# Kernel optimization log

Measured on AMD Instinct MI355X. Metric: run time of the kernel, lower is better.

Reference implementation:

```python
import jax, jax.numpy as jnp
import numpy as np

B, IN, OUT, E, CTX, DEMO = 32768, 512, 128, 16, 256, 16
HID = IN // 2
GATE_IN = CTX + IN + DEMO  # 784


def setup_inputs() -> dict:
    key = jax.random.key(0)
    ks = jax.random.split(key, 9)
    inp = {
        'x': jax.random.normal(ks[0], (B, IN), dtype=jnp.float32),
        'u': jax.random.normal(ks[1], (B, CTX), dtype=jnp.float32),
        'd': jax.random.normal(ks[2], (B, DEMO), dtype=jnp.float32),
        # gate Linear(GATE_IN -> E)
        'gate_W': jax.random.normal(ks[3], (E, GATE_IN), dtype=jnp.float32) * 0.02,
        'gate_b': jnp.zeros((E,), dtype=jnp.float32),
        # per-expert MLP: Linear(IN->HID), ReLU, Linear(HID->OUT); stacked over experts
        'W1': jax.random.normal(ks[4], (E, HID, IN), dtype=jnp.float32) * 0.02,
        'b1': jnp.zeros((E, HID), dtype=jnp.float32),
        'W2': jax.random.normal(ks[5], (E, OUT, HID), dtype=jnp.float32) * 0.02,
        'b2': jnp.zeros((E, OUT), dtype=jnp.float32),
    }
    return inp


def reference(x, u, d, gate_W, gate_b, W1, b1, W2, b2):
    # gate input = cat([u, x, d], dim=1)  -> [B, GATE_IN]
    g_in = jnp.concatenate([u, x, d], axis=1)
    gate_logits = g_in @ gate_W.T + gate_b            # [B, E]
    weights = jax.nn.softmax(gate_logits, axis=1)     # [B, E]
    # all-expert MLP as batched GEMMs
    h = jax.nn.relu(jnp.einsum('bi,ehi->beh', x, W1) + b1[None])   # [B, E, HID]
    expert_outputs = jnp.einsum('beh,eoh->beo', h, W2) + b2[None]  # [B, E, OUT]
    # mixture_mode == 'logits': weighted sum over experts
    out = jnp.einsum('be,beo->bo', weights, expert_outputs)        # [B, OUT]
    return out
```

## Files before the change

### kernel.cpp

```cpp
#include <hip/hip_runtime.h>

#define B_    32768
#define IN_   512
#define HID_  256
#define OUT_  128
#define E_    16
#define CTX_  256
#define DEMO_ 16
#define GIN_  784

typedef __attribute__((ext_vector_type(8))) short short8;
typedef __attribute__((ext_vector_type(4))) float floatx4;

__device__ __forceinline__ short f2bf(float x){
  unsigned u = __builtin_bit_cast(unsigned, x);
  u += 0x7FFFu + ((u >> 16) & 1u);
  return (short)(u >> 16);
}

__device__ __forceinline__ short8 pack8(float4 a, float4 b){
  short8 r;
  r[0]=f2bf(a.x); r[1]=f2bf(a.y); r[2]=f2bf(a.z); r[3]=f2bf(a.w);
  r[4]=f2bf(b.x); r[5]=f2bf(b.y); r[6]=f2bf(b.z); r[7]=f2bf(b.w);
  return r;
}

__device__ __forceinline__ void load_lds16(const short* g, short* l){
  __builtin_amdgcn_global_load_lds((const __attribute__((address_space(1))) void*)g,
                                   (__attribute__((address_space(3))) void*)l,
                                   16, 0, 0);
}

#define VMCNT8()  asm volatile("s_waitcnt vmcnt(8)"  ::: "memory")
#define VMCNT0()  asm volatile("s_waitcnt vmcnt(0)"  ::: "memory")
#define BAR() do{ asm volatile("" ::: "memory"); __builtin_amdgcn_s_barrier(); \
                  asm volatile("" ::: "memory"); }while(0)
#define LGKM0() do{ asm volatile("s_waitcnt lgkmcnt(0)" ::: "memory"); \
                    __builtin_amdgcn_sched_barrier(0); }while(0)

__device__ __forceinline__ void stage128x64(short* lds, const short* g, int gpitch, int tid){
  const int wvv = tid >> 6, ln = tid & 63;
  const int cb = ln & 7, rsub = ln >> 3;
  #pragma unroll
  for (int i = 0; i < 4; ++i){
    const int r0  = (wvv*4 + i)*8;
    const int row = r0 + rsub;
    const short* gp = g + (size_t)row*gpitch + ((cb ^ rsub) << 3);
    load_lds16(gp, lds + r0*64);
  }
}

__global__ void convert_kernel(const float* __restrict__ w1, const float* __restrict__ w2,
                               short* __restrict__ w1b, short* __restrict__ w2b){
  const int N2 = E_*HID_*IN_, N3 = E_*OUT_*HID_;
  const int total4 = (N2 + N3) >> 2;
  for (int i = blockIdx.x*blockDim.x + threadIdx.x; i < total4; i += gridDim.x*blockDim.x){
    int e4 = i << 2;
    const float* src; short* dst; int off;
    if (e4 < N2) { src = w1; dst = w1b; off = e4; }
    else         { src = w2; dst = w2b; off = e4 - N2; }
    float4 v = *(const float4*)(src + off);
    *(short4*)(dst + off) = make_short4(f2bf(v.x), f2bf(v.y), f2bf(v.z), f2bf(v.w));
  }
}

__global__ __launch_bounds__(256)
void gate_kernel(const float* __restrict__ x, const float* __restrict__ u,
                 const float* __restrict__ d, const float* __restrict__ gW,
                 const float* __restrict__ gb, short* __restrict__ xb,
                 float* __restrict__ wout){
  const int tid  = threadIdx.x;
  const int wave = tid >> 6, lane = tid & 63;
  const int l15  = lane & 15, quad = lane >> 4;
  const int row0 = blockIdx.x*64 + wave*16;
  const int rA   = row0 + l15;
  const int kq   = quad*8;

  floatx4 acc  = {0.f,0.f,0.f,0.f};
  floatx4 acc2 = {0.f,0.f,0.f,0.f};

  #pragma unroll
  for (int t = 0; t < 8; ++t){
    const float4 a0 = *(const float4*)&u[(size_t)rA*CTX_ + t*32 + kq];
    const float4 a1 = *(const float4*)&u[(size_t)rA*CTX_ + t*32 + kq + 4];
    const float4 b0 = *(const float4*)&gW[(size_t)l15*GIN_ + t*32 + kq];
    const float4 b1 = *(const float4*)&gW[(size_t)l15*GIN_ + t*32 + kq + 4];
    acc = __builtin_amdgcn_mfma_f32_16x16x32_bf16(pack8(a0,a1), pack8(b0,b1), acc, 0,0,0);
  }
  #pragma unroll
  for (int t = 0; t < 16; ++t){
    const float4 a0 = *(const float4*)&x[(size_t)rA*IN_ + t*32 + kq];
    const float4 a1 = *(const float4*)&x[(size_t)rA*IN_ + t*32 + kq + 4];
    const short8 af = pack8(a0, a1);
    *(short8*)&xb[(size_t)rA*IN_ + t*32 + kq] = af;
    const float4 b0 = *(const float4*)&gW[(size_t)l15*GIN_ + 256 + t*32 + kq];
    const float4 b1 = *(const float4*)&gW[(size_t)l15*GIN_ + 256 + t*32 + kq + 4];
    acc2 = __builtin_amdgcn_mfma_f32_16x16x32_bf16(af, pack8(b0,b1), acc2, 0,0,0);
  }
  {
    short8 af = {0,0,0,0,0,0,0,0}, bf = {0,0,0,0,0,0,0,0};
    if (quad < 2){
      const float4 a0 = *(const float4*)&d[(size_t)rA*DEMO_ + kq];
      const float4 a1 = *(const float4*)&d[(size_t)rA*DEMO_ + kq + 4];
      const float4 b0 = *(const float4*)&gW[(size_t)l15*GIN_ + 768 + kq];
      const float4 b1 = *(const float4*)&gW[(size_t)l15*GIN_ + 768 + kq + 4];
      af = pack8(a0,a1); bf = pack8(b0,b1);
    }
    acc = __builtin_amdgcn_mfma_f32_16x16x32_bf16(af, bf, acc, 0,0,0);
  }

  const float bias = gb[l15];
  #pragma unroll
  for (int r = 0; r < 4; ++r){
    float v = acc[r] + acc2[r] + bias;
    float m = v;
    #pragma unroll
    for (int s = 1; s <= 8; s <<= 1) m = fmaxf(m, __shfl_xor(m, s));
    const float p = __expf(v - m);
    float ssum = p;
    #pragma unroll
    for (int s = 1; s <= 8; s <<= 1) ssum += __shfl_xor(ssum, s);
    wout[(size_t)(row0 + quad*4 + r)*E_ + l15] = p / ssum;
  }
}

__global__ __launch_bounds__(256, 2)
void moe_kernel(const short* __restrict__ xb, const short* __restrict__ w1b,
                const short* __restrict__ w2b, const float* __restrict__ gatew,
                const float* __restrict__ b1g, const float* __restrict__ b2g,
                float* __restrict__ out){
  __shared__ alignas(16) char smem[65536];
  short* s_h  = (short*)smem;
  short* s_w2 = (short*)(smem + 32768);

  const int tid  = threadIdx.x;
  const int wv   = tid >> 6;
  const int lane = tid & 63;
  const int l15  = lane & 15;
  const int hi2  = lane >> 4;
  const int r7   = l15 & 7;
  const int h_off  = (wv >> 1) * 64;
  const int mb_off = (wv & 1) * 64;
  const int m_off  = (wv >> 1) * 64;
  const int o_off  = (wv & 1) * 64;
  const int blk_m0 = blockIdx.x * 128;
  const int eg = blockIdx.y;

  floatx4 oacc[4][4];
  #pragma unroll
  for (int a = 0; a < 4; ++a)
    #pragma unroll
    for (int b = 0; b < 4; ++b) oacc[a][b] = floatx4{0.f,0.f,0.f,0.f};

  #pragma unroll 1
  for (int ei = 0; ei < 4; ++ei){
    const int e = eg*4 + ei;
    float b2v[4];
    #pragma unroll
    for (int nt = 0; nt < 4; ++nt) b2v[nt] = b2g[e*OUT_ + o_off + nt*16 + l15];
    #pragma unroll
    for (int mt = 0; mt < 4; ++mt){
      #pragma unroll
      for (int r = 0; r < 4; ++r){
        const float wgt = gatew[(size_t)(blk_m0 + m_off + mt*16 + hi2*4 + r)*E_ + e];
        #pragma unroll
        for (int nt = 0; nt < 4; ++nt) oacc[mt][nt][r] += wgt * b2v[nt];
      }
    }
  }

  const short* xbase = xb + (size_t)blk_m0*IN_;

  #pragma unroll 1
  for (int ei = 0; ei < 4; ++ei){
    const int e = eg*4 + ei;
    #pragma unroll 1
    for (int half = 0; half < 2; ++half){
      const short* w1base = w1b + (size_t)(e*HID_ + half*128) * IN_;
      const short* w2base = w2b + (size_t)e*OUT_*HID_ + half*128;

      floatx4 g1[4][4];
      #pragma unroll
      for (int a = 0; a < 4; ++a)
        #pragma unroll
        for (int b = 0; b < 4; ++b) g1[a][b] = floatx4{0.f,0.f,0.f,0.f};

      stage128x64((short*)(smem +      0), xbase,  IN_, tid);
      stage128x64((short*)(smem + 16384), w1base, IN_, tid);

      #pragma unroll 1
      for (int kc = 0; kc < 8; ++kc){
        if (kc < 7){
          char* nb = smem + ((kc + 1) & 1)*32768;
          stage128x64((short*)nb,            xbase  + (kc+1)*64, IN_, tid);
          stage128x64((short*)(nb + 16384),  w1base + (kc+1)*64, IN_, tid);
          VMCNT8();
        } else {
          VMCNT0();
        }
        BAR();
        const short* buf = (const short*)(smem + (kc & 1)*32768);
        __builtin_amdgcn_s_setprio(1);
        #pragma unroll
        for (int ks = 0; ks < 2; ++ks){
          const int kb  = ks*4 + hi2;
          const int swz = (kb ^ r7) << 3;
          short8 af[4], bf[4];
          #pragma unroll
          for (int ht = 0; ht < 4; ++ht)
            af[ht] = *(const short8*)&buf[8192 + (h_off + ht*16 + l15)*64 + swz];
          #pragma unroll
          for (int mt = 0; mt < 4; ++mt)
            bf[mt] = *(const short8*)&buf[(mb_off + mt*16 + l15)*64 + swz];
          #pragma unroll
          for (int ht = 0; ht < 4; ++ht)
            #pragma unroll
            for (int mt = 0; mt < 4; ++mt)
              g1[ht][mt] = __builtin_amdgcn_mfma_f32_16x16x32_bf16(af[ht], bf[mt], g1[ht][mt], 0,0,0);
        }
        __builtin_amdgcn_s_setprio(0);
        LGKM0();
        BAR();
      }

      stage128x64(s_w2,        w2base,      HID_, tid);
      stage128x64(s_w2 + 8192, w2base + 64, HID_, tid);

      {
        float4 b1v[4];
        #pragma unroll
        for (int ht = 0; ht < 4; ++ht)
          b1v[ht] = *(const float4*)&b1g[e*HID_ + half*128 + h_off + ht*16 + hi2*4];
        float wgt[4];
        #pragma unroll
        for (int mt = 0; mt < 4; ++mt)
          wgt[mt] = gatew[(size_t)(blk_m0 + mb_off + mt*16 + l15)*E_ + e];
        #pragma unroll
        for (int ht = 0; ht < 4; ++ht){
          const float b1r[4] = {b1v[ht].x, b1v[ht].y, b1v[ht].z, b1v[ht].w};
          const int hb3 = 2*ht + (hi2 >> 1);
          #pragma unroll
          for (int mt = 0; mt < 4; ++mt){
            short4 pk;
            float v0 = fmaxf(g1[ht][mt][0] + b1r[0], 0.f) * wgt[mt];
            float v1 = fmaxf(g1[ht][mt][1] + b1r[1], 0.f) * wgt[mt];
            float v2 = fmaxf(g1[ht][mt][2] + b1r[2], 0.f) * wgt[mt];
            float v3 = fmaxf(g1[ht][mt][3] + b1r[3], 0.f) * wgt[mt];
            pk.x = f2bf(v0); pk.y = f2bf(v1); pk.z = f2bf(v2); pk.w = f2bf(v3);
            *(short4*)&s_h[(size_t)(mb_off + mt*16 + l15)*128 + h_off
                           + ((hb3 ^ r7) << 3) + (hi2 & 1)*4] = pk;
          }
        }
      }
      asm volatile("s_waitcnt vmcnt(0) lgkmcnt(0)" ::: "memory");
      __builtin_amdgcn_sched_barrier(0);
      BAR();

      __builtin_amdgcn_s_setprio(1);
      #pragma unroll
      for (int kc2 = 0; kc2 < 2; ++kc2){
        const short* wb = s_w2 + kc2*8192;
        #pragma unroll
        for (int ks = 0; ks < 2; ++ks){
          const int kb  = ks*4 + hi2;
          const int swz = (kb ^ r7) << 3;
          short8 af[4], bf[4];
          #pragma unroll
          for (int mt = 0; mt < 4; ++mt)
            af[mt] = *(const short8*)&s_h[(size_t)(m_off + mt*16 + l15)*128 + kc2*64 + swz];
          #pragma unroll
          for (int nt = 0; nt < 4; ++nt)
            bf[nt] = *(const short8*)&wb[(o_off + nt*16 + l15)*64 + swz];
          #pragma unroll
          for (int mt = 0; mt < 4; ++mt)
            #pragma unroll
            for (int nt = 0; nt < 4; ++nt)
              oacc[mt][nt] = __builtin_amdgcn_mfma_f32_16x16x32_bf16(af[mt], bf[nt], oacc[mt][nt], 0,0,0);
        }
      }
      __builtin_amdgcn_s_setprio(0);
      LGKM0();
      BAR();
    }
  }

  #pragma unroll
  for (int mt = 0; mt < 4; ++mt)
    #pragma unroll
    for (int nt = 0; nt < 4; ++nt)
      #pragma unroll
      for (int r = 0; r < 4; ++r)
        atomicAdd(&out[(size_t)(blk_m0 + m_off + mt*16 + hi2*4 + r)*OUT_ + o_off + nt*16 + l15],
                  oacc[mt][nt][r]);
}

extern "C" void kernel_launch(void* const* d_in, const int* in_sizes, int n_in,
                              void* d_out, int out_size, void* d_ws, size_t ws_size,
                              hipStream_t stream){
  const float* x  = (const float*)d_in[0];
  const float* u  = (const float*)d_in[1];
  const float* dd = (const float*)d_in[2];
  const float* gW = (const float*)d_in[3];
  const float* gb = (const float*)d_in[4];
  const float* W1 = (const float*)d_in[5];
  const float* b1 = (const float*)d_in[6];
  const float* W2 = (const float*)d_in[7];
  const float* b2 = (const float*)d_in[8];
  float* out = (float*)d_out;

  short* xb  = (short*)d_ws;
  short* w1b = xb  + (size_t)B_*IN_;
  short* w2b = w1b + (size_t)E_*HID_*IN_;
  float* gw  = (float*)(w2b + (size_t)E_*OUT_*HID_);

  hipMemsetAsync(d_out, 0, (size_t)B_*OUT_*sizeof(float), stream);
  hipLaunchKernelGGL(convert_kernel, dim3(1024), dim3(256), 0, stream, W1, W2, w1b, w2b);
  hipLaunchKernelGGL(gate_kernel, dim3(B_/64), dim3(256), 0, stream, x, u, dd, gW, gb, xb, gw);
  hipLaunchKernelGGL(moe_kernel, dim3(B_/128, 4), dim3(256), 0, stream,
                     xb, w1b, w2b, gw, b1, b2, out);
  (void)in_sizes; (void)n_in; (void)out_size; (void)ws_size;
}
```

Before: 371.5 us.

## Merge weight conversion and gate into one prep kernel with split-K waves

Folds the weight bf16 conversion kernel into the gate kernel as extra blocks, so the two independent prep jobs run in a single launch and can overlap. The gate work is also split along K across pairs of waves, each covering 16 rows, and the partial sums are reduced through LDS. This doubles the gate block count and parallelism at the cost of one barrier and a small shared buffer. It aims to cut one launch gap and to better saturate memory bandwidth during the prep phase.

```diff
diff --git a/kernel.cpp b/kernel.cpp
--- a/kernel.cpp
+++ b/kernel.cpp
@@ -8,6 +8,9 @@
 #define CTX_  256
 #define DEMO_ 16
 #define GIN_  784
+
+#define GATEB_ 1024
+#define CONVB_ 512
 
 typedef __attribute__((ext_vector_type(8))) short short8;
 typedef __attribute__((ext_vector_type(4))) float floatx4;
@@ -50,77 +53,101 @@
   }
 }
 
-__global__ void convert_kernel(const float* __restrict__ w1, const float* __restrict__ w2,
-                               short* __restrict__ w1b, short* __restrict__ w2b){
-  const int N2 = E_*HID_*IN_, N3 = E_*OUT_*HID_;
-  const int total4 = (N2 + N3) >> 2;
-  for (int i = blockIdx.x*blockDim.x + threadIdx.x; i < total4; i += gridDim.x*blockDim.x){
-    int e4 = i << 2;
-    const float* src; short* dst; int off;
-    if (e4 < N2) { src = w1; dst = w1b; off = e4; }
-    else         { src = w2; dst = w2b; off = e4 - N2; }
-    float4 v = *(const float4*)(src + off);
-    *(short4*)(dst + off) = make_short4(f2bf(v.x), f2bf(v.y), f2bf(v.z), f2bf(v.w));
-  }
-}
-
 __global__ __launch_bounds__(256)
-void gate_kernel(const float* __restrict__ x, const float* __restrict__ u,
+void prep_kernel(const float* __restrict__ x, const float* __restrict__ u,
                  const float* __restrict__ d, const float* __restrict__ gW,
-                 const float* __restrict__ gb, short* __restrict__ xb,
-                 float* __restrict__ wout){
+                 const float* __restrict__ gb,
+                 const float* __restrict__ w1, const float* __restrict__ w2,
+                 short* __restrict__ xb, short* __restrict__ w1b,
+                 short* __restrict__ w2b, float* __restrict__ wout){
+  if (blockIdx.x >= GATEB_){
+    const int N2 = E_*HID_*IN_, N3 = E_*OUT_*HID_;
+    const int total4 = (N2 + N3) >> 2;
+    for (int i = (blockIdx.x - GATEB_)*blockDim.x + threadIdx.x; i < total4;
+         i += CONVB_*blockDim.x){
+      int e4 = i << 2;
+      const float* src; short* dst; int off;
+      if (e4 < N2) { src = w1; dst = w1b; off = e4; }
+      else         { src = w2; dst = w2b; off = e4 - N2; }
+      float4 v = *(const float4*)(src + off);
+      *(short4*)(dst + off) = make_short4(f2bf(v.x), f2bf(v.y), f2bf(v.z), f2bf(v.w));
+    }
+    return;
+  }
+
+  __shared__ float pacc[2][64][4];
+
   const int tid  = threadIdx.x;
   const int wave = tid >> 6, lane = tid & 63;
+  const int pair = wave >> 1, role = wave & 1;
   const int l15  = lane & 15, quad = lane >> 4;
-  const int row0 = blockIdx.x*64 + wave*16;
+  const int row0 = blockIdx.x*32 + pair*16;
   const int rA   = row0 + l15;
   const int kq   = quad*8;
 
-  floatx4 acc  = {0.f,0.f,0.f,0.f};
-  floatx4 acc2 = {0.f,0.f,0.f,0.f};
-
-  #pragma unroll
-  for (int t = 0; t < 8; ++t){
-    const float4 a0 = *(const float4*)&u[(size_t)rA*CTX_ + t*32 + kq];
-    const float4 a1 = *(const float4*)&u[(size_t)rA*CTX_ + t*32 + kq + 4];
-    const float4 b0 = *(const float4*)&gW[(size_t)l15*GIN_ + t*32 + kq];
-    const float4 b1 = *(const float4*)&gW[(size_t)l15*GIN_ + t*32 + kq + 4];
-    acc = __builtin_amdgcn_mfma_f32_16x16x32_bf16(pack8(a0,a1), pack8(b0,b1), acc, 0,0,0);
-  }
-  #pragma unroll
-  for (int t = 0; t < 16; ++t){
-    const float4 a0 = *(const float4*)&x[(size_t)rA*IN_ + t*32 + kq];
-    const float4 a1 = *(const float4*)&x[(size_t)rA*IN_ + t*32 + kq + 4];
-    const short8 af = pack8(a0, a1);
-    *(short8*)&xb[(size_t)rA*IN_ + t*32 + kq] = af;
-    const float4 b0 = *(const float4*)&gW[(size_t)l15*GIN_ + 256 + t*32 + kq];
-    const float4 b1 = *(const float4*)&gW[(size_t)l15*GIN_ + 256 + t*32 + kq + 4];
-    acc2 = __builtin_amdgcn_mfma_f32_16x16x32_bf16(af, pack8(b0,b1), acc2, 0,0,0);
-  }
-  {
-    short8 af = {0,0,0,0,0,0,0,0}, bf = {0,0,0,0,0,0,0,0};
-    if (quad < 2){
-      const float4 a0 = *(const float4*)&d[(size_t)rA*DEMO_ + kq];
-      const float4 a1 = *(const float4*)&d[(size_t)rA*DEMO_ + kq + 4];
-      const float4 b0 = *(const float4*)&gW[(size_t)l15*GIN_ + 768 + kq];
-      const float4 b1 = *(const float4*)&gW[(size_t)l15*GIN_ + 768 + kq + 4];
-      af = pack8(a0,a1); bf = pack8(b0,b1);
-    }
-    acc = __builtin_amdgcn_mfma_f32_16x16x32_bf16(af, bf, acc, 0,0,0);
-  }
-
-  const float bias = gb[l15];
-  #pragma unroll
-  for (int r = 0; r < 4; ++r){
-    float v = acc[r] + acc2[r] + bias;
-    float m = v;
-    #pragma unroll
-    for (int s = 1; s <= 8; s <<= 1) m = fmaxf(m, __shfl_xor(m, s));
-    const float p = __expf(v - m);
-    float ssum = p;
-    #pragma unroll
-    for (int s = 1; s <= 8; s <<= 1) ssum += __shfl_xor(ssum, s);
-    wout[(size_t)(row0 + quad*4 + r)*E_ + l15] = p / ssum;
+  floatx4 acc = {0.f,0.f,0.f,0.f};
+
+  if (role == 0){
+    #pragma unroll
+    for (int t = 0; t < 8; ++t){
+      const float4 a0 = *(const float4*)&u[(size_t)rA*CTX_ + t*32 + kq];
+      const float4 a1 = *(const float4*)&u[(size_t)rA*CTX_ + t*32 + kq + 4];
+      const float4 b0 = *(const float4*)&gW[(size_t)l15*GIN_ + t*32 + kq];
+      const float4 b1 = *(const float4*)&gW[(size_t)l15*GIN_ + t*32 + kq + 4];
+      acc = __builtin_amdgcn_mfma_f32_16x16x32_bf16(pack8(a0,a1), pack8(b0,b1), acc, 0,0,0);
+    }
+    #pragma unroll
+    for (int t = 0; t < 8; ++t){
+      const float4 a0 = *(const float4*)&x[(size_t)rA*IN_ + t*32 + kq];
+      const float4 a1 = *(const float4*)&x[(size_t)rA*IN_ + t*32 + kq + 4];
+      const short8 af = pack8(a0, a1);
+      *(short8*)&xb[(size_t)rA*IN_ + t*32 + kq] = af;
+      const float4 b0 = *(const float4*)&gW[(size_t)l15*GIN_ + 256 + t*32 + kq];
+      const float4 b1 = *(const float4*)&gW[(size_t)l15*GIN_ + 256 + t*32 + kq + 4];
+      acc = __builtin_amdgcn_mfma_f32_16x16x32_bf16(af, pack8(b0,b1), acc, 0,0,0);
+    }
+  } else {
+    #pragma unroll
+    for (int t = 8; t < 16; ++t){
+      const float4 a0 = *(const float4*)&x[(size_t)rA*IN_ + t*32 + kq];
+      const float4 a1 = *(const float4*)&x[(size_t)rA*IN_ + t*32 + kq + 4];
+      const short8 af = pack8(a0, a1);
+      *(short8*)&xb[(size_t)rA*IN_ + t*32 + kq] = af;
+      const float4 b0 = *(const float4*)&gW[(size_t)l15*GIN_ + 256 + t*32 + kq];
+      const float4 b1 = *(const float4*)&gW[(size_t)l15*GIN_ + 256 + t*32 + kq + 4];
+      acc = __builtin_amdgcn_mfma_f32_16x16x32_bf16(af, pack8(b0,b1), acc, 0,0,0);
+    }
+    {
+      short8 af = {0,0,0,0,0,0,0,0}, bf = {0,0,0,0,0,0,0,0};
+      if (quad < 2){
+        const float4 a0 = *(const float4*)&d[(size_t)rA*DEMO_ + kq];
+        const float4 a1 = *(const float4*)&d[(size_t)rA*DEMO_ + kq + 4];
+        const float4 b0 = *(const float4*)&gW[(size_t)l15*GIN_ + 768 + kq];
+        const float4 b1 = *(const float4*)&gW[(size_t)l15*GIN_ + 768 + kq + 4];
+        af = pack8(a0,a1); bf = pack8(b0,b1);
+      }
+      acc = __builtin_amdgcn_mfma_f32_16x16x32_bf16(af, bf, acc, 0,0,0);
+    }
+    #pragma unroll
+    for (int r = 0; r < 4; ++r) pacc[pair][lane][r] = acc[r];
+  }
+
+  __syncthreads();
+
+  if (role == 0){
+    const float bias = gb[l15];
+    #pragma unroll
+    for (int r = 0; r < 4; ++r){
+      float v = acc[r] + pacc[pair][lane][r] + bias;
+      float m = v;
+      #pragma unroll
+      for (int s = 1; s <= 8; s <<= 1) m = fmaxf(m, __shfl_xor(m, s));
+      const float p = __expf(v - m);
+      float ssum = p;
+      #pragma unroll
+      for (int s = 1; s <= 8; s <<= 1) ssum += __shfl_xor(ssum, s);
+      wout[(size_t)(row0 + quad*4 + r)*E_ + l15] = p / ssum;
+    }
   }
 }
 
@@ -314,8 +341,8 @@
   float* gw  = (float*)(w2b + (size_t)E_*OUT_*HID_);
 
   hipMemsetAsync(d_out, 0, (size_t)B_*OUT_*sizeof(float), stream);
-  hipLaunchKernelGGL(convert_kernel, dim3(1024), dim3(256), 0, stream, W1, W2, w1b, w2b);
-  hipLaunchKernelGGL(gate_kernel, dim3(B_/64), dim3(256), 0, stream, x, u, dd, gW, gb, xb, gw);
+  hipLaunchKernelGGL(prep_kernel, dim3(GATEB_ + CONVB_), dim3(256), 0, stream,
+                     x, u, dd, gW, gb, W1, W2, xb, w1b, w2b, gw);
   hipLaunchKernelGGL(moe_kernel, dim3(B_/128, 4), dim3(256), 0, stream,
                      xb, w1b, w2b, gw, b1, b2, out);
   (void)in_sizes; (void)n_in; (void)out_size; (void)ws_size;
```

Measured after the change: 379.4 us. +2.1%, slower.
